# Optimization experiments

Hardware: AMD Instinct MI355X
Metric: run time of the kernel (lower is better)

## Reference

```python
import jax, jax.numpy as jnp
import numpy as np

# ---- constants from __init__ ----
DT = 1.0
NX, NY = 192, 192
SRC_X, SRC_Y = 40, 96
PX = jnp.array([160, 160, 160])
PY = jnp.array([48, 96, 144])
PML_N, PML_P, PML_MAX = 20, 4.0, 3.0
C0, C1 = 1.0, 0.9
H = DT * 2.01 / 1.0  # grid spacing


def make_b():
    """PML damping profile b(x,y), [NX, NY]."""
    v = (PML_MAX * np.linspace(0.0, 1.0, PML_N + 1) ** PML_P).astype(np.float32)
    bx = np.zeros((NX, NY), np.float32)
    bx[: PML_N + 1, :] = v[::-1, None]
    bx[NX - PML_N - 1 :, :] = v[:, None]
    by = np.zeros((NX, NY), np.float32)
    by[:, : PML_N + 1] = v[::-1][None, :]
    by[:, NY - PML_N - 1 :] = v[None, :]
    return jnp.asarray(np.sqrt(bx ** 2 + by ** 2))


def _conv3(img, kern):
    # img [B,1,H,W], kern [1,1,3,3], 'same' padding
    return jax.lax.conv_general_dilated(
        img, kern, (1, 1), ((1, 1), (1, 1)),
        dimension_numbers=("NCHW", "OIHW", "NCHW"))


def _proj(x, eta=0.5, beta=100.0):
    return (jnp.tanh(beta * eta) + jnp.tanh(beta * (x - eta))) / (
        jnp.tanh(beta * eta) + jnp.tanh(beta * (1.0 - eta)))


def setup_inputs() -> dict:
    key = jax.random.key(0)
    k1, k2 = jax.random.split(key)
    x = jax.random.normal(k1, (4, 256), dtype=jnp.float32)  # [batch, T]
    rho = jax.random.uniform(k2, (NX, NY), dtype=jnp.float32)
    # clip_pml_rho(): rho[b != 0] = 0 for binarized model (applied at init)
    rho = jnp.where(make_b() != 0, 0.0, rho)
    return {"x": x, "rho": rho}


def reference(x, rho):
    b = make_b()
    lpf_k = jnp.array([[[[0.0, 0.125, 0.0], [0.125, 0.5, 0.125], [0.0, 0.125, 0.0]]]], jnp.float32)
    lap_k = (H ** -2) * jnp.array([[[[0.0, 1.0, 0.0], [1.0, -4.0, 1.0], [0.0, 1.0, 0.0]]]], jnp.float32)
    A1 = 1.0 / (DT ** -2 + b * 0.5 / DT)
    A2 = 2.0 * DT ** -2
    A3 = DT ** -2 - b * 0.5 / DT

    # binarized wave-speed field c(rho): LPF then tanh projection
    lpf_rho = _conv3(rho[None, None], lpf_k)[0, 0]
    c = C0 + (C1 - C0) * _proj(lpf_rho)
    c2 = c * c

    B = x.shape[0]
    y0 = jnp.zeros((B, NX, NY), x.dtype)

    def step(carry, xi):
        y1, y2 = carry
        lap = _conv3(y1[:, None], lap_k)[:, 0]            # [B,NX,NY]
        y = A1 * (A2 * y1 - A3 * y2 + c2 * lap)
        y = y.at[:, SRC_X, SRC_Y].add(xi)                 # source injection
        return (y, y1), y[:, PX, PY]                      # emit probe values [B,P]

    _, probes = jax.lax.scan(step, (y0, y0), x.T)         # probes [T,B,P]

    # integrate_probe_points: sum |y|^2 over time, normalize per batch
    I = jnp.sum(probes ** 2, axis=0)                      # [B,P]
    return I / jnp.sum(I, axis=1, keepdims=True)
```

## Files before the change

### kernel.cpp

```cpp
#include <hip/hip_runtime.h>
#include <math.h>

#define NXY    192
#define CELLS  (NXY*NXY)
#define NBATCH 4
#define NSTEPS 256
#define TCH    16
#define NCHUNK (NSTEPS/TCH)
#define TPB    512
#define NW     8
#define RPL    5
#define OUTR   6
#define NBLKS  256

#define K3_OFF (16*CELLS)
#define Q_OFF  (K3_OFF + CELLS)
#define I_OFF  (Q_OFF + CELLS)

typedef float v2f __attribute__((ext_vector_type(2)));

__device__ __forceinline__ float dpp_up1(float v) {
    int r = __builtin_amdgcn_update_dpp(0, __builtin_bit_cast(int, v),
                                        0x138, 0xf, 0xf, true);
    return __builtin_bit_cast(float, r);
}
__device__ __forceinline__ float dpp_dn1(float v) {
    int r = __builtin_amdgcn_update_dpp(0, __builtin_bit_cast(int, v),
                                        0x130, 0xf, 0xf, true);
    return __builtin_bit_cast(float, r);
}

__device__ __forceinline__ float pml_prof(int i) {
    int t;
    if (i <= 20)            t = 20 - i;
    else if (i >= NXY - 21) t = i - (NXY - 21);
    else                    return 0.0f;
    float u  = (float)t * 0.05f;
    float u2 = u * u;
    return 3.0f * u2 * u2;
}

__global__ void setup_k(const float* __restrict__ rho, float* __restrict__ ws) {
    int idx    = blockIdx.x * blockDim.x + threadIdx.x;
    int stride = gridDim.x * blockDim.x;
    for (int k = idx; k < 8 * CELLS; k += stride) ws[k] = 0.0f;
    const float IH2 = (float)(1.0 / (2.01 * 2.01));
    for (int k = idx; k < CELLS; k += stride) {
        int i = k / NXY, j = k % NXY;
        float r0 = rho[k];
        float ru = (i > 0)       ? rho[k - NXY] : 0.0f;
        float rd = (i < NXY - 1) ? rho[k + NXY] : 0.0f;
        float rl = (j > 0)       ? rho[k - 1]   : 0.0f;
        float rr2 = (j < NXY - 1) ? rho[k + 1]  : 0.0f;
        float lpf = 0.5f * r0 + 0.125f * ((ru + rd) + (rl + rr2));
        float p   = 0.5f * (1.0f + tanhf(100.0f * (lpf - 0.5f)));
        float c   = 1.0f - 0.1f * p;
        float c2h = c * c * IH2;
        float bx = pml_prof(i), by = pml_prof(j);
        float bb = sqrtf(bx * bx + by * by);
        float a1 = 1.0f / (1.0f + 0.5f * bb);
        ws[K3_OFF + k] = a1 * c2h;
        ws[Q_OFF  + k] = 1.0f - 2.0f * a1;
    }
    if (idx < 12) ws[I_OFF + idx] = 0.0f;
}

__global__ __launch_bounds__(TPB, 1)
void chunk_k(const float* __restrict__ x, float* __restrict__ ws, int chunk) {
    int blk = blockIdx.x;
    int b  = blk / 64;
    int r_ = blk % 64;
    int bi = r_ >> 1, cj = r_ & 1;
    int I0 = OUTR * bi - 17;
    int J0 = 96 * cj - 16;
    int t  = threadIdx.x;
    int w  = t >> 6;
    int l  = t & 63;
    int row0 = I0 + RPL * w;
    int gj   = J0 + 2 * l;

    __shared__ v2f hb[2][2][NW + 2][64];
    for (int k = t; k < 2 * 2 * (NW + 2) * 64; k += TPB)
        ((v2f*)hb)[k] = (v2f){0.f, 0.f};

    float xv[TCH];
    int xbase = b * NSTEPS + chunk * TCH;
#pragma unroll
    for (int i = 0; i < TCH; i++) xv[i] = x[xbase + i];

    const float* kg = ws + K3_OFF;
    const float* qg = ws + Q_OFF;
    int pin = chunk & 1, pout = pin ^ 1;
    const float* curg  = ws + ((pin  * 2 + 0) * NBATCH + b) * CELLS;
    const float* prvg  = ws + ((pin  * 2 + 1) * NBATCH + b) * CELLS;
    float*       ncurg = ws + ((pout * 2 + 0) * NBATCH + b) * CELLS;
    float*       nprvg = ws + ((pout * 2 + 1) * NBATCH + b) * CELLS;

    v2f yc[RPL], yp[RPL], Qa[RPL], Ka[RPL];
    bool cok = (gj >= 0 && gj < NXY);
#pragma unroll
    for (int r = 0; r < RPL; r++) {
        int gi = row0 + r;
        bool ok = cok && gi >= 0 && gi < NXY;
        v2f kv = {0.f,0.f}, qv = {0.f,0.f}, cv = {0.f,0.f}, pv = {0.f,0.f};
        if (ok) {
            int idx = gi * NXY + gj;
            kv = *(const v2f*)(kg + idx);
            qv = *(const v2f*)(qg + idx);
            cv = *(const v2f*)(curg + idx);
            pv = *(const v2f*)(prvg + idx);
        }
        yc[r] = cv; yp[r] = pv; Ka[r] = kv; Qa[r] = qv;
    }

    int sr = 40 - I0, sc = 96 - J0;
    bool wave_src = (sr >= RPL * w) && (sr < RPL * w + RPL);
    int src_rl = sr - RPL * w;
    float srcm = (2 * l == sc) ? 1.f : 0.f;

    int pcl = 2 * l + J0;
    bool wave_prb = (bi == 26) && (w == 4);
    const int prb_rl = 1;
    bool is_prb = (cj == 0) ? (pcl == 48) : (pcl == 96 || pcl == 144);
    float prbm = is_prb ? 1.f : 0.f;
    float pacc = 0.f;

    v2f uph, dnh;

#define ROWC(CUR, PRV, rr_, UP, DN, XSV, YN) do {                              \
    v2f cv = CUR[rr_];                                                         \
    float lf0 = dpp_up1(cv.y);                                                 \
    float rt1 = dpp_dn1(cv.x);                                                 \
    v2f h = (v2f){lf0, rt1} + __builtin_shufflevector(cv, cv, 1, 0);           \
    v2f S = ((UP) + (DN)) + h;                                                 \
    YN = cv + Qa[rr_] * (PRV[rr_] - cv) + Ka[rr_] * (S - 4.0f * cv);           \
    if (wave_src && (rr_) == src_rl) YN.x += srcm * (XSV);                     \
    if (wave_prb && (rr_) == prb_rl) { float q = prbm * YN.x; pacc += q * YN.x; } \
} while (0)

#define STEP(CUR, PRV, PH, SIDX) do {                                          \
    v2f t0, t4;                                                                \
    ROWC(CUR, PRV, 0, uph,    CUR[1], xv[SIDX], t0);                           \
    ROWC(CUR, PRV, 4, CUR[3], dnh,    xv[SIDX], t4);                           \
    hb[PH][0][w + 1][l] = t0;                                                  \
    hb[PH][1][w + 1][l] = t4;                                                  \
    PRV[0] = t0; PRV[4] = t4;                                                  \
    _Pragma("unroll")                                                          \
    for (int r = 1; r <= 3; r++) {                                             \
        v2f y;                                                                 \
        ROWC(CUR, PRV, r, CUR[r - 1], CUR[r + 1], xv[SIDX], y);                \
        PRV[r] = y;                                                            \
    }                                                                          \
    __syncthreads();                                                           \
    uph = hb[PH][1][w][l];                                                     \
    dnh = hb[PH][0][w + 2][l];                                                 \
} while (0)

    hb[0][0][w + 1][l] = yc[0];
    hb[0][1][w + 1][l] = yc[4];
    __syncthreads();
    uph = hb[0][1][w][l];
    dnh = hb[0][0][w + 2][l];

#pragma unroll
    for (int s2 = 0; s2 < TCH / 2; s2++) {
        STEP(yc, yp, 1, 2 * s2);
        STEP(yp, yc, 0, 2 * s2 + 1);
    }
#undef STEP
#undef ROWC

#pragma unroll
    for (int r = 0; r < RPL; r++) {
        int gi = row0 + r;
        if (gi >= OUTR * bi && gi < OUTR * bi + OUTR && l >= 8 && l < 56) {
            int idx = gi * NXY + gj;
            *(v2f*)(ncurg + idx) = yc[r];
            *(v2f*)(nprvg + idx) = yp[r];
        }
    }
    if (wave_prb && is_prb)
        ws[I_OFF + b * 3 + (pcl / 48 - 1)] += pacc;
}

__global__ void final_k(const float* __restrict__ ws, float* __restrict__ out) {
    int t = threadIdx.x;
    if (t < 12) {
        const float* I = ws + I_OFF;
        int b = t / 3;
        float s = I[3 * b] + I[3 * b + 1] + I[3 * b + 2];
        out[t] = I[t] / s;
    }
}

extern "C" void kernel_launch(void* const* d_in, const int* in_sizes, int n_in,
                              void* d_out, int out_size, void* d_ws, size_t ws_size,
                              hipStream_t stream) {
    const float* x   = (const float*)d_in[0];
    const float* rho = (const float*)d_in[1];
    float* ws  = (float*)d_ws;
    float* out = (float*)d_out;

    setup_k<<<256, 256, 0, stream>>>(rho, ws);
    for (int c = 0; c < NCHUNK; c++)
        chunk_k<<<NBLKS, TPB, 0, stream>>>(x, ws, c);
    final_k<<<1, 64, 0, stream>>>(ws, out);
}
```

Measured before the change: 201.4 us.

## Exchange two-row halos per barrier to halve block synchronizations

Each wave now keeps a 9-row register window: its 5 owned rows plus 2 ghost rows on each side. It exchanges a deeper halo (two current rows and one previous row per side) through shared memory once per pair of time steps instead of once per step, redundantly recomputing the ghost rows to do so. This halves the __syncthreads count in the time loop, at the cost of extra redundant row computations, more registers, and more LDS traffic per exchange.

```diff
diff --git a/kernel.cpp b/kernel.cpp
--- a/kernel.cpp
+++ b/kernel.cpp
@@ -76,12 +76,15 @@
     int t  = threadIdx.x;
     int w  = t >> 6;
     int l  = t & 63;
-    int row0 = I0 + RPL * w;
+    int row0 = I0 + RPL * w - 2;
     int gj   = J0 + 2 * l;
 
-    __shared__ v2f hb[2][2][NW + 2][64];
-    for (int k = t; k < 2 * 2 * (NW + 2) * 64; k += TPB)
-        ((v2f*)hb)[k] = (v2f){0.f, 0.f};
+    __shared__ v2f T[2][NW + 1][3][64];
+    __shared__ v2f B[2][NW + 1][3][64];
+    for (int k = t; k < 2 * (NW + 1) * 3 * 64; k += TPB) {
+        ((v2f*)T)[k] = (v2f){0.f, 0.f};
+        ((v2f*)B)[k] = (v2f){0.f, 0.f};
+    }
 
     float xv[TCH];
     int xbase = b * NSTEPS + chunk * TCH;
@@ -96,82 +99,93 @@
     float*       ncurg = ws + ((pout * 2 + 0) * NBATCH + b) * CELLS;
     float*       nprvg = ws + ((pout * 2 + 1) * NBATCH + b) * CELLS;
 
-    v2f yc[RPL], yp[RPL], Qa[RPL], Ka[RPL];
     bool cok = (gj >= 0 && gj < NXY);
-#pragma unroll
-    for (int r = 0; r < RPL; r++) {
+
+    v2f yc[9], yp[9], Ka[9], Qa[9];
+#pragma unroll
+    for (int r = 2; r <= 6; r++) {
         int gi = row0 + r;
         bool ok = cok && gi >= 0 && gi < NXY;
-        v2f kv = {0.f,0.f}, qv = {0.f,0.f}, cv = {0.f,0.f}, pv = {0.f,0.f};
+        v2f cv = {0.f,0.f}, pv = {0.f,0.f};
+        if (ok) {
+            int idx = gi * NXY + gj;
+            cv = *(const v2f*)(curg + idx);
+            pv = *(const v2f*)(prvg + idx);
+        }
+        yc[r] = cv; yp[r] = pv;
+    }
+#pragma unroll
+    for (int r = 1; r <= 7; r++) {
+        int gi = row0 + r;
+        bool ok = cok && gi >= 0 && gi < NXY;
+        v2f kv = {0.f,0.f}, qv = {0.f,0.f};
         if (ok) {
             int idx = gi * NXY + gj;
             kv = *(const v2f*)(kg + idx);
             qv = *(const v2f*)(qg + idx);
-            cv = *(const v2f*)(curg + idx);
-            pv = *(const v2f*)(prvg + idx);
         }
-        yc[r] = cv; yp[r] = pv; Ka[r] = kv; Qa[r] = qv;
-    }
-
-    int sr = 40 - I0, sc = 96 - J0;
-    bool wave_src = (sr >= RPL * w) && (sr < RPL * w + RPL);
-    int src_rl = sr - RPL * w;
+        Ka[r] = kv; Qa[r] = qv;
+    }
+
+    int src_r = 40 - row0;
+    int sc = 96 - J0;
     float srcm = (2 * l == sc) ? 1.f : 0.f;
 
     int pcl = 2 * l + J0;
+    int prb_r = 160 - row0;
     bool wave_prb = (bi == 26) && (w == 4);
-    const int prb_rl = 1;
     bool is_prb = (cj == 0) ? (pcl == 48) : (pcl == 96 || pcl == 144);
     float prbm = is_prb ? 1.f : 0.f;
     float pacc = 0.f;
 
-    v2f uph, dnh;
-
-#define ROWC(CUR, PRV, rr_, UP, DN, XSV, YN) do {                              \
+#define ROWC(CUR, PRV, rr_, XSV) do {                                         \
     v2f cv = CUR[rr_];                                                         \
     float lf0 = dpp_up1(cv.y);                                                 \
     float rt1 = dpp_dn1(cv.x);                                                 \
     v2f h = (v2f){lf0, rt1} + __builtin_shufflevector(cv, cv, 1, 0);           \
-    v2f S = ((UP) + (DN)) + h;                                                 \
-    YN = cv + Qa[rr_] * (PRV[rr_] - cv) + Ka[rr_] * (S - 4.0f * cv);           \
-    if (wave_src && (rr_) == src_rl) YN.x += srcm * (XSV);                     \
-    if (wave_prb && (rr_) == prb_rl) { float q = prbm * YN.x; pacc += q * YN.x; } \
+    v2f S = (CUR[rr_ - 1] + CUR[rr_ + 1]) + h;                                 \
+    v2f yn = cv + Qa[rr_] * (PRV[rr_] - cv) + Ka[rr_] * (S - 4.0f * cv);       \
+    if ((rr_) == src_r) yn.x += srcm * (XSV);                                  \
+    if (wave_prb && (rr_) == prb_r) { float q = prbm * yn.x; pacc += q * yn.x; } \
+    PRV[rr_] = yn;                                                             \
 } while (0)
 
-#define STEP(CUR, PRV, PH, SIDX) do {                                          \
-    v2f t0, t4;                                                                \
-    ROWC(CUR, PRV, 0, uph,    CUR[1], xv[SIDX], t0);                           \
-    ROWC(CUR, PRV, 4, CUR[3], dnh,    xv[SIDX], t4);                           \
-    hb[PH][0][w + 1][l] = t0;                                                  \
-    hb[PH][1][w + 1][l] = t4;                                                  \
-    PRV[0] = t0; PRV[4] = t4;                                                  \
-    _Pragma("unroll")                                                          \
-    for (int r = 1; r <= 3; r++) {                                             \
-        v2f y;                                                                 \
-        ROWC(CUR, PRV, r, CUR[r - 1], CUR[r + 1], xv[SIDX], y);                \
-        PRV[r] = y;                                                            \
-    }                                                                          \
-    __syncthreads();                                                           \
-    uph = hb[PH][1][w][l];                                                     \
-    dnh = hb[PH][0][w + 2][l];                                                 \
-} while (0)
-
-    hb[0][0][w + 1][l] = yc[0];
-    hb[0][1][w + 1][l] = yc[4];
     __syncthreads();
-    uph = hb[0][1][w][l];
-    dnh = hb[0][0][w + 2][l];
-
-#pragma unroll
-    for (int s2 = 0; s2 < TCH / 2; s2++) {
-        STEP(yc, yp, 1, 2 * s2);
-        STEP(yp, yc, 0, 2 * s2 + 1);
-    }
-#undef STEP
+
+#pragma unroll
+    for (int c = 0; c < TCH / 2; c++) {
+        int p = c & 1;
+        T[p][w + 1][0][l] = yc[5];
+        T[p][w + 1][1][l] = yc[6];
+        T[p][w + 1][2][l] = yp[6];
+        B[p][w][0][l]     = yc[2];
+        B[p][w][1][l]     = yc[3];
+        B[p][w][2][l]     = yp[2];
+        __syncthreads();
+        yc[0] = T[p][w][0][l];
+        yc[1] = T[p][w][1][l];
+        yp[1] = T[p][w][2][l];
+        yc[7] = B[p][w + 1][0][l];
+        yc[8] = B[p][w + 1][1][l];
+        yp[7] = B[p][w + 1][2][l];
+
+        ROWC(yc, yp, 3, xv[2 * c]);
+        ROWC(yc, yp, 4, xv[2 * c]);
+        ROWC(yc, yp, 5, xv[2 * c]);
+        ROWC(yc, yp, 2, xv[2 * c]);
+        ROWC(yc, yp, 6, xv[2 * c]);
+        ROWC(yc, yp, 1, xv[2 * c]);
+        ROWC(yc, yp, 7, xv[2 * c]);
+        ROWC(yp, yc, 2, xv[2 * c + 1]);
+        ROWC(yp, yc, 3, xv[2 * c + 1]);
+        ROWC(yp, yc, 5, xv[2 * c + 1]);
+        ROWC(yp, yc, 6, xv[2 * c + 1]);
+        ROWC(yp, yc, 4, xv[2 * c + 1]);
+    }
 #undef ROWC
 
 #pragma unroll
-    for (int r = 0; r < RPL; r++) {
+    for (int r = 2; r <= 6; r++) {
         int gi = row0 + r;
         if (gi >= OUTR * bi && gi < OUTR * bi + OUTR && l >= 8 && l < 56) {
             int idx = gi * NXY + gj;
```

New measurement: 222.1 us. +10.3%, slower.
